# Performance work log

Measured on AMD Instinct MI355X. Metric: run time of the kernel, lower is better.

The kernel has to match this reference:

```python
import jax, jax.numpy as jnp
import numpy as np

B, S, H = 2, 2048, 2048
NH, NKV, HD = 16, 4, 128
ROPE_BASE = 10000.0


def setup_inputs() -> dict:
    key = jax.random.key(0)
    ks = jax.random.split(key, 5)
    x = jax.random.normal(ks[0], (B, S, H), dtype=jnp.float32)
    position_ids = jnp.arange(S, dtype=jnp.int64 if jax.config.jax_enable_x64 else jnp.int32).reshape(1, S)
    # Linear weights stored as [in, out] (equivalent to torch weight.T)
    sc = 1.0 / np.sqrt(H)
    Wq = jax.random.normal(ks[1], (H, NH * HD), dtype=jnp.float32) * sc
    Wk = jax.random.normal(ks[2], (H, NKV * HD), dtype=jnp.float32) * sc
    Wv = jax.random.normal(ks[3], (H, NKV * HD), dtype=jnp.float32) * sc
    Wo = jax.random.normal(ks[4], (NH * HD, H), dtype=jnp.float32) * (1.0 / np.sqrt(NH * HD))
    return {"x": x, "position_ids": position_ids, "Wq": Wq, "Wk": Wk, "Wv": Wv, "Wo": Wo}


def _rope(q, k, position_ids):
    # q: [B,S,NH,HD], k: [B,S,NKV,HD]; Llama-style half-split RoPE
    half = HD // 2
    inv_freq = 1.0 / (ROPE_BASE ** (jnp.arange(0, half, dtype=jnp.float32) * 2.0 / HD))
    ang = position_ids.astype(jnp.float32)[..., None] * inv_freq  # [b,S,half]
    cos = jnp.concatenate([jnp.cos(ang), jnp.cos(ang)], axis=-1)[:, :, None, :]  # [b,S,1,HD]
    sin = jnp.concatenate([jnp.sin(ang), jnp.sin(ang)], axis=-1)[:, :, None, :]

    def rot_half(t):
        t1, t2 = t[..., :half], t[..., half:]
        return jnp.concatenate([-t2, t1], axis=-1)

    return q * cos + rot_half(q) * sin, k * cos + rot_half(k) * sin


def reference(x, position_ids, Wq, Wk, Wv, Wo):
    b, s, _ = x.shape
    q = (x @ Wq).reshape(b, s, NH, HD)
    k = (x @ Wk).reshape(b, s, NKV, HD)
    v = (x @ Wv).reshape(b, s, NKV, HD)
    q, k = _rope(q, k, position_ids)
    reps = NH // NKV
    k = jnp.repeat(k, reps, axis=2)  # repeat_interleave on head dim
    v = jnp.repeat(v, reps, axis=2)
    q = q.transpose(0, 2, 1, 3)  # [b,h,s,d]
    k = k.transpose(0, 2, 1, 3)
    v = v.transpose(0, 2, 1, 3)
    scores = jnp.einsum('bhqd,bhkd->bhqk', q, k) / jnp.sqrt(jnp.float32(HD))
    causal = jnp.triu(jnp.ones((s, s), dtype=bool), k=1)
    scores = jnp.where(causal, -jnp.inf, scores)
    attn = jax.nn.softmax(scores.astype(jnp.float32), axis=-1).astype(q.dtype)
    out = jnp.einsum('bhqk,bhkd->bhqd', attn, v)
    out = out.transpose(0, 2, 1, 3).reshape(b, s, NH * HD)
    return out @ Wo
```

## Files before the change

kernel.cpp:

```cpp
#include <hip/hip_runtime.h>
#include <stdint.h>

typedef unsigned short u16;
typedef __attribute__((ext_vector_type(8))) short short8;
typedef __attribute__((ext_vector_type(4))) short short4v;
typedef __attribute__((ext_vector_type(4))) float floatx4;

#define S_LEN 2048
#define NQKV 3072

#if __has_builtin(__builtin_amdgcn_exp2f)
#define EXP2F __builtin_amdgcn_exp2f
#else
#define EXP2F exp2f
#endif

__device__ inline float bf2f(u16 u) {
  union { uint32_t u; float f; } v; v.u = ((uint32_t)u) << 16; return v.f;
}
__device__ inline u16 f2bf(float f) {
  union { float f; uint32_t u; } v; v.f = f;
  uint32_t r = v.u + 0x7fffu + ((v.u >> 16) & 1u);
  return (u16)(r >> 16);
}
__device__ inline void gl2lds16(const u16* g, u16* l) {
  __builtin_amdgcn_global_load_lds((const __attribute__((address_space(1))) uint32_t*)g,
                                   (__attribute__((address_space(3))) uint32_t*)l, 16, 0, 0);
}

__global__ void prep_k(const float* __restrict__ x, u16* __restrict__ Xb,
                       const float* __restrict__ Wq, const float* __restrict__ Wk,
                       const float* __restrict__ Wv, const float* __restrict__ Wo,
                       u16* __restrict__ WT, u16* __restrict__ WoT,
                       const int* __restrict__ pos, float2* __restrict__ rtab) {
  __shared__ u16 tile[32][33];
  const int b = blockIdx.x, t = threadIdx.x;
  if (b < 8192) {
    int i = b * 256 + t;
    float4 v = ((const float4*)x)[i];
    ushort4 o;
    o.x = f2bf(v.x); o.y = f2bf(v.y); o.z = f2bf(v.z); o.w = f2bf(v.w);
    ((ushort4*)Xb)[i] = o;
    return;
  }
  if (b >= 18432) {
    int i = (b - 18432) * 256 + t;
    int s = i >> 6, d = i & 63;
    float freq = __expf(-(float)d * 0.015625f * 9.210340371976184f);
    float ang = (float)pos[s] * freq;
    rtab[i] = make_float2(cosf(ang), sinf(ang));
    return;
  }
  int wb = b - 8192;
  const float* src; u16* dst; int bx, by;
  if (wb < 4096)      { src = Wq; dst = WT;                       bx = wb & 63;  by = wb >> 6; }
  else if (wb < 5120) { src = Wk; dst = WT + (size_t)2048 * 2048; bx = (wb - 4096) & 15; by = (wb - 4096) >> 4; }
  else if (wb < 6144) { src = Wv; dst = WT + (size_t)2560 * 2048; bx = (wb - 5120) & 15; by = (wb - 5120) >> 4; }
  else                { src = Wo; dst = WoT;                      bx = (wb - 6144) & 63; by = (wb - 6144) >> 6; }
  const int N = (wb >= 4096 && wb < 6144) ? 512 : 2048;
  int n0 = bx * 32, k0 = by * 32;
  int tx = t & 31, ty = t >> 5;
#pragma unroll
  for (int i = 0; i < 4; i++)
    tile[ty + 8 * i][tx] = f2bf(src[(size_t)(k0 + ty + 8 * i) * N + n0 + tx]);
  __syncthreads();
#pragma unroll
  for (int i = 0; i < 4; i++)
    dst[(size_t)(n0 + ty + 8 * i) * 2048 + k0 + tx] = tile[tx][ty + 8 * i];
}

template <bool OUTF32>
__global__ __launch_bounds__(256) void gemm_bt(const u16* __restrict__ A, const u16* __restrict__ Bt,
                                               void* __restrict__ Cv, int M, int N, int K) {
  __shared__ u16 As[128 * 32];
  __shared__ u16 Bs[128 * 32];
  const int m0 = blockIdx.y * 128, n0 = blockIdx.x * 128;
  const int t = threadIdx.x, w = t >> 6, lane = t & 63;
  const int quad = lane >> 4, l16 = lane & 15;
  const int wm = (w >> 1) * 64, wn = (w & 1) * 64;
  const int lrow = lane >> 2, lk = (lane & 3) * 8;
  floatx4 acc[4][4] = {};
  for (int k0 = 0; k0 < K; k0 += 32) {
#pragma unroll
    for (int c = 2 * w; c <= 2 * w + 1; ++c) {
      int row = c * 16 + lrow;
      gl2lds16(A + (size_t)(m0 + row) * K + k0 + lk, As + c * 512 + lane * 8);
      gl2lds16(Bt + (size_t)(n0 + row) * K + k0 + lk, Bs + c * 512 + lane * 8);
    }
    __syncthreads();
    short8 a[4], b[4];
#pragma unroll
    for (int mt = 0; mt < 4; mt++) a[mt] = *(const short8*)(As + (wm + mt * 16 + l16) * 32 + quad * 8);
#pragma unroll
    for (int nt = 0; nt < 4; nt++) b[nt] = *(const short8*)(Bs + (wn + nt * 16 + l16) * 32 + quad * 8);
#pragma unroll
    for (int mt = 0; mt < 4; mt++)
#pragma unroll
      for (int nt = 0; nt < 4; nt++)
        acc[mt][nt] = __builtin_amdgcn_mfma_f32_16x16x32_bf16(a[mt], b[nt], acc[mt][nt], 0, 0, 0);
    __syncthreads();
  }
#pragma unroll
  for (int mt = 0; mt < 4; mt++)
#pragma unroll
    for (int nt = 0; nt < 4; nt++)
#pragma unroll
      for (int r = 0; r < 4; r++) {
        int row = m0 + wm + mt * 16 + quad * 4 + r;
        int col = n0 + wn + nt * 16 + l16;
        if (OUTF32)
          ((float*)Cv)[(size_t)row * N + col] = acc[mt][nt][r];
        else
          ((u16*)Cv)[(size_t)row * N + col] = f2bf(acc[mt][nt][r]);
      }
}

__global__ __launch_bounds__(512, 2) void gemm256_k(const u16* __restrict__ A,
                                                    const u16* __restrict__ Bt,
                                                    u16* __restrict__ C,
                                                    const float2* __restrict__ rtab,
                                                    int N, int K) {
  __shared__ u16 SM[65536];
  u16* const AlB = SM;
  u16* const BlB = SM + 32768;
  const int TN = N >> 8;
  int flat = blockIdx.x;
  const int cpx = gridDim.x >> 3;
  flat = (flat & 7) * cpx + (flat >> 3);
  const int m0 = (flat / TN) << 8, n0 = (flat % TN) << 8;
  const int t = threadIdx.x, w = t >> 6, lane = t & 63;
  const int quad = lane >> 4, l16 = lane & 15;
  const int wm = w >> 2, wn = w & 3;
  const int sr = t >> 3, sl = t & 7;
  floatx4 acc[2][2][4][2] = {};
  const int NKT = K >> 6;

  const int ra_l = wm * 64 + l16;
  const int rb_l = wn * 16 + l16;

#pragma unroll
  for (int round = 0; round < 2; round++) {
    int r = round * 64 + sr;
    int so = (sl ^ (r & 7)) << 3;
    gl2lds16(A + (size_t)(m0 + r) * K + so, AlB + round * 4096 + t * 8);
    gl2lds16(Bt + (size_t)(n0 + r) * K + so, BlB + round * 4096 + t * 8);
    gl2lds16(Bt + (size_t)(n0 + 128 + r) * K + so, BlB + 8192 + round * 4096 + t * 8);
    gl2lds16(A + (size_t)(m0 + 128 + r) * K + so, AlB + 8192 + round * 4096 + t * 8);
  }
  asm volatile("s_waitcnt vmcnt(0)" ::: "memory");
  __builtin_amdgcn_s_barrier();

  short8 af[4][2];
  short8 bf[2][2][2];

  for (int kt = 0; kt < NKT; kt++) {
    const int c = kt & 1;
    const u16* Ab = AlB + c * 16384;
    const u16* Bb = BlB + c * 16384;
    u16* An = AlB + (c ^ 1) * 16384;
    u16* Bn = BlB + (c ^ 1) * 16384;
    const int k1 = (kt + 1) << 6;
    const bool pf = (kt + 1 < NKT);
#pragma unroll
    for (int ph = 0; ph < 4; ph++) {
      const int mh = (ph >> 1);
      const int nh = (ph == 1 || ph == 2) ? 1 : 0;
      if (ph == 0 || ph == 1) {
#pragma unroll
        for (int nt = 0; nt < 2; nt++) {
          int rb = rb_l + nt * 64;
          const u16* base = Bb + nh * 8192 + rb * 64;
#pragma unroll
          for (int ks = 0; ks < 2; ks++)
            bf[nh][nt][ks] = *(const short8*)(base + (((ks * 4 + quad) ^ (rb & 7)) << 3));
        }
      }
      if (ph == 0 || ph == 2) {
#pragma unroll
        for (int mt = 0; mt < 4; mt++) {
          int ra = ra_l + mt * 16;
          const u16* base = Ab + mh * 8192 + ra * 64;
#pragma unroll
          for (int ks = 0; ks < 2; ks++)
            af[mt][ks] = *(const short8*)(base + (((ks * 4 + quad) ^ (ra & 7)) << 3));
        }
      }
      if (pf) {
        const u16* G;
        u16* L;
        int rbase;
        if (ph == 0)      { G = A;  L = An;        rbase = m0; }
        else if (ph == 1) { G = Bt; L = Bn;        rbase = n0; }
        else if (ph == 2) { G = Bt; L = Bn + 8192; rbase = n0 + 128; }
        else              { G = A;  L = An + 8192; rbase = m0 + 128; }
#pragma unroll
        for (int round = 0; round < 2; round++) {
          int r = round * 64 + sr;
          gl2lds16(G + (size_t)(rbase + r) * K + k1 + ((sl ^ (r & 7)) << 3),
                   L + round * 4096 + t * 8);
        }
      }
      __builtin_amdgcn_s_barrier();
      __builtin_amdgcn_s_setprio(1);
#pragma unroll
      for (int mt = 0; mt < 4; mt++)
#pragma unroll
        for (int nt = 0; nt < 2; nt++)
#pragma unroll
          for (int ks = 0; ks < 2; ks++)
            acc[mh][nh][mt][nt] =
                __builtin_amdgcn_mfma_f32_16x16x32_bf16(af[mt][ks], bf[nh][nt][ks], acc[mh][nh][mt][nt], 0, 0, 0);
      __builtin_amdgcn_s_setprio(0);
      if (ph != 2) {
        if (pf) asm volatile("s_waitcnt vmcnt(4)" ::: "memory");
        else    asm volatile("s_waitcnt vmcnt(0)" ::: "memory");
      }
      __builtin_amdgcn_s_barrier();
    }
  }
  if (n0 < 2560) {
    const int dloc = wn * 16 + l16;
#pragma unroll
    for (int mh = 0; mh < 2; mh++)
#pragma unroll
      for (int mt = 0; mt < 4; mt++)
#pragma unroll
        for (int r = 0; r < 4; r++) {
          int row = m0 + mh * 128 + wm * 64 + mt * 16 + quad * 4 + r;
          float2 cs = rtab[(row & (S_LEN - 1)) * 64 + dloc];
#pragma unroll
          for (int nh = 0; nh < 2; nh++) {
            float a0 = acc[mh][nh][mt][0][r], a1 = acc[mh][nh][mt][1][r];
            float o0 = a0 * cs.x - a1 * cs.y;
            float o1 = a1 * cs.x + a0 * cs.y;
            int colb = n0 + nh * 128 + wn * 16 + l16;
            C[(size_t)row * N + colb]      = f2bf(o0);
            C[(size_t)row * N + colb + 64] = f2bf(o1);
          }
        }
  } else {
    const int bbv = m0 >> 11, m0loc = m0 & 2047;
    const int kvbase = (n0 - 2560) >> 7;
#pragma unroll
    for (int mh = 0; mh < 2; mh++)
#pragma unroll
      for (int nh = 0; nh < 2; nh++)
#pragma unroll
        for (int mt = 0; mt < 4; mt++)
#pragma unroll
          for (int pair = 0; pair < 2; pair++) {
            int lrow = mh * 128 + wm * 64 + mt * 16 + quad * 4;
            int lcol = nh * 128 + wn * 16 + l16 + pair * 64;
            short4v v4 = { (short)f2bf(acc[mh][nh][mt][pair][0]),
                           (short)f2bf(acc[mh][nh][mt][pair][1]),
                           (short)f2bf(acc[mh][nh][mt][pair][2]),
                           (short)f2bf(acc[mh][nh][mt][pair][3]) };
            *(short4v*)(SM + lcol * 256 + (lrow ^ ((lcol & 15) << 3))) = v4;
          }
    asm volatile("s_waitcnt lgkmcnt(0)" ::: "memory");
    __builtin_amdgcn_s_barrier();
#pragma unroll
    for (int it = 0; it < 16; it++) {
      int u = it * 512 + t;
      int key0 = (u & 31) * 8, lcol = u >> 5;
      short8 v = *(const short8*)(SM + lcol * 256 + (key0 ^ ((lcol & 15) << 3)));
      int d = lcol & 127, kvh = kvbase + (lcol >> 7);
      int key = m0loc + key0;
      *(short8*)(C + (size_t)(bbv * 2048 + kvh * 512 + d * 4 + (key >> 9)) * N + 2560 + (key & 511)) = v;
    }
  }
}

__global__ __launch_bounds__(256) void attn_k(const u16* __restrict__ qkv,
                                              u16* __restrict__ ctx) {
  __shared__ u16 Kl[2][64 * 128];
  __shared__ u16 Vl[2][128 * 64];
  const int f = blockIdx.x;
  const int p = f >> 5;
  const int hb = f & 31;
  const int h = hb & 15, bb = hb >> 4;
  const int kvh = h >> 2;
  const int t = threadIdx.x, w = t >> 6, lane = t & 63;
  const int quad = lane >> 4, l16 = lane & 15;
  const int sx = l16 & 7;
  const int kslot = lane & 15;
  const int vd0 = w * 32 + (lane >> 3);
  const int vslot = lane & 7;
  const int grow0 = (w & 1) * 4 + (w >> 1) * 32 + quad;
  const size_t rowbase = (size_t)bb * S_LEN;
  const u16* Kg0 = qkv + rowbase * NQKV + 2048 + kvh * 128;
  const u16* Vg0 = qkv + (rowbase + kvh * 512) * NQKV + 2560;
  const float c2 = 0.12751744f;
  short8 onesf = {16256, 16256, 16256, 16256, 16256, 16256, 16256, 16256};

  for (int phase = 0; phase < 2; phase++) {
    const int qt = phase ? p : 31 - p;
    const int rw = qt * 64 + w * 16;
    const int qrow = rw + l16;

    short8 qf[4];
#pragma unroll
    for (int ks = 0; ks < 4; ks++)
      qf[ks] = *(const short8*)(qkv + (rowbase + rw + l16) * NQKV + h * 128 + ks * 32 + quad * 8);

    floatx4 acc[8] = {};
    floatx4 accl = {0.f, 0.f, 0.f, 0.f};

    __syncthreads();
    {
#pragma unroll
      for (int ii = 0; ii < 4; ii++) {
        int p7 = (quad + 4 * ii) & 7;
        int grow = grow0 + 8 * ii;
        gl2lds16(Kg0 + (size_t)grow * NQKV + ((kslot ^ p7) * 8),
                 &Kl[0][0] + w * 2048 + ii * 512 + lane * 8);
      }
#pragma unroll
      for (int ii = 0; ii < 4; ii++) {
        int d = vd0 + ii * 8;
        int s8 = (vslot ^ (d & 7)) * 8;
        gl2lds16(Vg0 + (size_t)(d * 4) * NQKV + s8,
                 &Vl[0][0] + w * 2048 + ii * 512 + lane * 8);
      }
    }

    for (int kb = 0; kb <= qt; kb++) {
      const int cur = kb & 1;
      __builtin_amdgcn_s_barrier();
      if (kb < qt) {
        const int kn = kb + 1;
        const u16* Kg = Kg0 + (size_t)kn * 64 * NQKV;
        u16* KlN = &Kl[cur ^ 1][0];
        u16* VlN = &Vl[cur ^ 1][0];
#pragma unroll
        for (int ii = 0; ii < 4; ii++) {
          int p7 = (quad + 4 * ii) & 7;
          int grow = grow0 + 8 * ii;
          gl2lds16(Kg + (size_t)grow * NQKV + ((kslot ^ p7) * 8),
                   KlN + w * 2048 + ii * 512 + lane * 8);
        }
#pragma unroll
        for (int ii = 0; ii < 4; ii++) {
          int d = vd0 + ii * 8;
          int s8 = (vslot ^ (d & 7)) * 8;
          gl2lds16(Vg0 + (size_t)(d * 4 + (kn >> 3)) * NQKV + (kn & 7) * 64 + s8,
                   VlN + w * 2048 + ii * 512 + lane * 8);
        }
        asm volatile("s_waitcnt vmcnt(8)" ::: "memory");
      } else {
        asm volatile("s_waitcnt vmcnt(0)" ::: "memory");
      }
      __builtin_amdgcn_s_barrier();
      const u16* KlB = &Kl[cur][0];
      const u16* VlB = &Vl[cur][0];

      floatx4 sc[4];
      __builtin_amdgcn_s_setprio(1);
#pragma unroll
      for (int nt = 0; nt < 4; nt++) {
        const u16* Krow = KlB + (nt * 16 + l16) * 128;
        short8 kf[4];
#pragma unroll
        for (int ks = 0; ks < 4; ks++)
          kf[ks] = *(const short8*)(Krow + (((ks * 4 + quad) ^ sx) * 8));
        floatx4 s = {0.f, 0.f, 0.f, 0.f};
#pragma unroll
        for (int ks = 0; ks < 4; ks++) s = __builtin_amdgcn_mfma_f32_16x16x32_bf16(kf[ks], qf[ks], s, 0, 0, 0);
        sc[nt] = s;
      }
      __builtin_amdgcn_s_setprio(0);
      const bool diag = (kb == qt);
      uint32_t pw[8];
#pragma unroll
      for (int nt = 0; nt < 4; nt++) {
        uint32_t w0 = 0, w1 = 0;
#pragma unroll
        for (int r = 0; r < 4; r++) {
          float e = EXP2F(sc[nt][r] * c2);
          if (diag) {
            int keyg = kb * 64 + quad * 8 + (nt & 1) * 4 + (nt >> 1) * 32 + r;
            if (keyg > qrow) e = 0.f;
          }
          uint32_t b = __float_as_uint(e) >> 16;
          if (r == 0) w0 = b;
          else if (r == 1) w0 |= b << 16;
          else if (r == 2) w1 = b;
          else w1 |= b << 16;
        }
        pw[nt * 2] = w0;
        pw[nt * 2 + 1] = w1;
      }
      union { short8 v; uint32_t u[4]; } pu0, pu1;
      pu0.u[0] = pw[0]; pu0.u[1] = pw[1]; pu0.u[2] = pw[2]; pu0.u[3] = pw[3];
      pu1.u[0] = pw[4]; pu1.u[1] = pw[5]; pu1.u[2] = pw[6]; pu1.u[3] = pw[7];
      const short8 pf0 = pu0.v, pf1 = pu1.v;

      __builtin_amdgcn_s_setprio(1);
      accl = __builtin_amdgcn_mfma_f32_16x16x32_bf16(pf0, onesf, accl, 0, 0, 0);
      accl = __builtin_amdgcn_mfma_f32_16x16x32_bf16(pf1, onesf, accl, 0, 0, 0);
#pragma unroll
      for (int nto = 0; nto < 8; nto++) {
        const u16* Vrow = VlB + (nto * 16 + l16) * 64;
        short8 vf0 = *(const short8*)(Vrow + ((quad ^ sx) * 8));
        short8 vf1 = *(const short8*)(Vrow + (((quad + 4) ^ sx) * 8));
        acc[nto] = __builtin_amdgcn_mfma_f32_16x16x32_bf16(pf0, vf0, acc[nto], 0, 0, 0);
        acc[nto] = __builtin_amdgcn_mfma_f32_16x16x32_bf16(pf1, vf1, acc[nto], 0, 0, 0);
      }
      __builtin_amdgcn_s_setprio(0);
    }
#pragma unroll
    for (int r = 0; r < 4; r++) {
      float inv = 1.0f / accl[r];
      int rowg = rw + quad * 4 + r;
#pragma unroll
      for (int nto = 0; nto < 8; nto++) {
        int col = h * 128 + nto * 16 + l16;
        ctx[(rowbase + rowg) * 2048 + col] = f2bf(acc[nto][r] * inv);
      }
    }
  }
}

extern "C" void kernel_launch(void* const* d_in, const int* in_sizes, int n_in,
                              void* d_out, int out_size, void* d_ws, size_t ws_size,
                              hipStream_t stream) {
  const float* x  = (const float*)d_in[0];
  const int* pos  = (const int*)d_in[1];
  const float* Wq = (const float*)d_in[2];
  const float* Wk = (const float*)d_in[3];
  const float* Wv = (const float*)d_in[4];
  const float* Wo = (const float*)d_in[5];
  float* out = (float*)d_out;
  char* ws = (char*)d_ws;
  u16* Xb  = (u16*)(ws);
  u16* WT  = (u16*)(ws + 16777216);
  u16* WoT = (u16*)(ws + 29360128);
  u16* QKV = (u16*)(ws + 37748736);
  u16* CTX = (u16*)(ws + 62914560);
  float2* rtab = (float2*)(ws + 62914560);

  hipLaunchKernelGGL(prep_k, dim3(18944), dim3(256), 0, stream, x, Xb, Wq, Wk, Wv, Wo, WT, WoT, pos, rtab);

  hipLaunchKernelGGL(gemm256_k, dim3(192), dim3(512), 0, stream, Xb, WT, QKV, rtab, 3072, 2048);
  hipLaunchKernelGGL(attn_k, dim3(512), dim3(256), 0, stream, QKV, CTX);
  hipLaunchKernelGGL(HIP_KERNEL_NAME(gemm_bt<true>), dim3(16, 32), dim3(256), 0, stream,
                     CTX, WoT, (void*)out, 4096, 2048, 2048);
}
```

Before: 284.0 us.

## Rewrite output projection GEMM with double-buffered LDS, swizzle, and XCD remap

Replaces the simple 128x128 output-projection GEMM with a version that double-buffers K tiles of 64 in LDS, overlapping global-to-LDS loads with MFMA compute through vmcnt waits. The LDS layout is XOR-swizzled to avoid bank conflicts, and block indices are remapped across the 8 XCDs for better L2 locality. It also raises wave priority around the MFMA block. The cost is more LDS per block (64KB), which may limit occupancy.

New measurement: 272.6 us. 1.04x faster.

```diff
diff --git a/kernel.cpp b/kernel.cpp
--- a/kernel.cpp
+++ b/kernel.cpp
@@ -69,36 +69,80 @@
     dst[(size_t)(n0 + ty + 8 * i) * 2048 + k0 + tx] = tile[tx][ty + 8 * i];
 }
 
-template <bool OUTF32>
-__global__ __launch_bounds__(256) void gemm_bt(const u16* __restrict__ A, const u16* __restrict__ Bt,
-                                               void* __restrict__ Cv, int M, int N, int K) {
-  __shared__ u16 As[128 * 32];
-  __shared__ u16 Bs[128 * 32];
-  const int m0 = blockIdx.y * 128, n0 = blockIdx.x * 128;
+__global__ __launch_bounds__(256) void gemm128_k(const u16* __restrict__ A,
+                                                 const u16* __restrict__ Bt,
+                                                 float* __restrict__ C, int M, int N, int K) {
+  __shared__ u16 Al[2][8192];
+  __shared__ u16 Bl[2][8192];
+  const int TN = N >> 7;
+  int flat = blockIdx.x;
+  const int cpx = gridDim.x >> 3;
+  flat = (flat & 7) * cpx + (flat >> 3);
+  const int m0 = (flat / TN) << 7, n0 = (flat % TN) << 7;
   const int t = threadIdx.x, w = t >> 6, lane = t & 63;
   const int quad = lane >> 4, l16 = lane & 15;
-  const int wm = (w >> 1) * 64, wn = (w & 1) * 64;
-  const int lrow = lane >> 2, lk = (lane & 3) * 8;
+  const int wm = w >> 1, wn = w & 1;
+  const int sr = t >> 3, sl = t & 7;
   floatx4 acc[4][4] = {};
-  for (int k0 = 0; k0 < K; k0 += 32) {
-#pragma unroll
-    for (int c = 2 * w; c <= 2 * w + 1; ++c) {
-      int row = c * 16 + lrow;
-      gl2lds16(A + (size_t)(m0 + row) * K + k0 + lk, As + c * 512 + lane * 8);
-      gl2lds16(Bt + (size_t)(n0 + row) * K + k0 + lk, Bs + c * 512 + lane * 8);
-    }
-    __syncthreads();
-    short8 a[4], b[4];
-#pragma unroll
-    for (int mt = 0; mt < 4; mt++) a[mt] = *(const short8*)(As + (wm + mt * 16 + l16) * 32 + quad * 8);
-#pragma unroll
-    for (int nt = 0; nt < 4; nt++) b[nt] = *(const short8*)(Bs + (wn + nt * 16 + l16) * 32 + quad * 8);
+  const int NKT = K >> 6;
+  const int ra_l = wm * 64 + l16;
+  const int rb_l = wn * 64 + l16;
+
+#pragma unroll
+  for (int round = 0; round < 4; round++) {
+    int r = round * 32 + sr;
+    int so = (sl ^ (r & 7)) << 3;
+    gl2lds16(A + (size_t)(m0 + r) * K + so, &Al[0][0] + round * 2048 + t * 8);
+    gl2lds16(Bt + (size_t)(n0 + r) * K + so, &Bl[0][0] + round * 2048 + t * 8);
+  }
+  asm volatile("s_waitcnt vmcnt(0)" ::: "memory");
+  __builtin_amdgcn_s_barrier();
+
+  for (int kt = 0; kt < NKT; kt++) {
+    const int cur = kt & 1;
+    __builtin_amdgcn_s_barrier();
+    if (kt + 1 < NKT) {
+      const int k1 = (kt + 1) << 6;
+#pragma unroll
+      for (int round = 0; round < 4; round++) {
+        int r = round * 32 + sr;
+        int so = (sl ^ (r & 7)) << 3;
+        gl2lds16(A + (size_t)(m0 + r) * K + k1 + so, &Al[cur ^ 1][0] + round * 2048 + t * 8);
+        gl2lds16(Bt + (size_t)(n0 + r) * K + k1 + so, &Bl[cur ^ 1][0] + round * 2048 + t * 8);
+      }
+      asm volatile("s_waitcnt vmcnt(8)" ::: "memory");
+    } else {
+      asm volatile("s_waitcnt vmcnt(0)" ::: "memory");
+    }
+    __builtin_amdgcn_s_barrier();
+    const u16* Ab = &Al[cur][0];
+    const u16* Bb = &Bl[cur][0];
+    short8 af[4][2], bf[4][2];
+#pragma unroll
+    for (int mt = 0; mt < 4; mt++) {
+      int ra = ra_l + mt * 16;
+      const u16* base = Ab + ra * 64;
+#pragma unroll
+      for (int ks = 0; ks < 2; ks++)
+        af[mt][ks] = *(const short8*)(base + (((ks * 4 + quad) ^ (ra & 7)) << 3));
+    }
+#pragma unroll
+    for (int nt = 0; nt < 4; nt++) {
+      int rb = rb_l + nt * 16;
+      const u16* base = Bb + rb * 64;
+#pragma unroll
+      for (int ks = 0; ks < 2; ks++)
+        bf[nt][ks] = *(const short8*)(base + (((ks * 4 + quad) ^ (rb & 7)) << 3));
+    }
+    __builtin_amdgcn_s_setprio(1);
 #pragma unroll
     for (int mt = 0; mt < 4; mt++)
 #pragma unroll
       for (int nt = 0; nt < 4; nt++)
-        acc[mt][nt] = __builtin_amdgcn_mfma_f32_16x16x32_bf16(a[mt], b[nt], acc[mt][nt], 0, 0, 0);
-    __syncthreads();
+#pragma unroll
+        for (int ks = 0; ks < 2; ks++)
+          acc[mt][nt] = __builtin_amdgcn_mfma_f32_16x16x32_bf16(af[mt][ks], bf[nt][ks], acc[mt][nt], 0, 0, 0);
+    __builtin_amdgcn_s_setprio(0);
   }
 #pragma unroll
   for (int mt = 0; mt < 4; mt++)
@@ -106,12 +150,9 @@
     for (int nt = 0; nt < 4; nt++)
 #pragma unroll
       for (int r = 0; r < 4; r++) {
-        int row = m0 + wm + mt * 16 + quad * 4 + r;
-        int col = n0 + wn + nt * 16 + l16;
-        if (OUTF32)
-          ((float*)Cv)[(size_t)row * N + col] = acc[mt][nt][r];
-        else
-          ((u16*)Cv)[(size_t)row * N + col] = f2bf(acc[mt][nt][r]);
+        int row = m0 + wm * 64 + mt * 16 + quad * 4 + r;
+        int col = n0 + wn * 64 + nt * 16 + l16;
+        C[(size_t)row * N + col] = acc[mt][nt][r];
       }
 }
 
@@ -443,6 +484,5 @@
 
   hipLaunchKernelGGL(gemm256_k, dim3(192), dim3(512), 0, stream, Xb, WT, QKV, rtab, 3072, 2048);
   hipLaunchKernelGGL(attn_k, dim3(512), dim3(256), 0, stream, QKV, CTX);
-  hipLaunchKernelGGL(HIP_KERNEL_NAME(gemm_bt<true>), dim3(16, 32), dim3(256), 0, stream,
-                     CTX, WoT, (void*)out, 4096, 2048, 2048);
-}
+  hipLaunchKernelGGL(gemm128_k, dim3(512), dim3(256), 0, stream, CTX, WoT, out, 4096, 2048, 2048);
+}
```
